# Optimization experiments

Hardware: AMD Instinct MI355X
Metric: run time of the kernel (lower is better)

Reference implementation:

```python
import jax, jax.numpy as jnp
import numpy as np

EPS = 1e-7
POS_THR = 0.5   # max_iou assigner positive threshold
NEG_THR = 0.4   # max_iou assigner negative threshold
ALPHA, GAMMA = 0.25, 2.0  # focal loss defaults


def _rand_boxes(key, shape):
    k1, k2 = jax.random.split(key)
    c = jax.random.uniform(k1, shape + (2,), minval=0.05, maxval=0.95)
    wh = jax.random.uniform(k2, shape + (2,), minval=0.02, maxval=0.3)
    return jnp.concatenate([jnp.clip(c - wh / 2, 0, 1), jnp.clip(c + wh / 2, 0, 1)], -1)


def _grid_anchors():
    # 3 anchor sizes per cell on 80x80, 40x40, 20x20 grids -> 25200 anchors, normalized coords
    boxes = []
    for g, sizes in [(80, (0.04, 0.08, 0.12)), (40, (0.1, 0.2, 0.3)), (20, (0.25, 0.45, 0.65))]:
        c = (np.arange(g, dtype=np.float32) + 0.5) / g
        cx, cy = np.meshgrid(c, c)
        for s in sizes:
            boxes.append(np.stack([cx - s / 2, cy - s / 2, cx + s / 2, cy + s / 2], -1).reshape(-1, 4))
    return jnp.asarray(np.concatenate(boxes, 0), dtype=jnp.float32)


def setup_inputs() -> dict:
    key = jax.random.key(0)
    ks = jax.random.split(key, 6)
    N, P, A, C = 32, 100, 25200, 80
    labels = jax.random.randint(ks[0], (N, P), 0, C)
    y_true = jax.nn.one_hot(labels, C, dtype=jnp.float32)
    bbox_true = _rand_boxes(ks[1], (N, P))
    valid = (jnp.arange(P)[None, :] < 30).astype(jnp.float32)  # 30 real boxes, rest zero-padded
    bbox_true = bbox_true * valid[..., None]
    conf_pred = jax.random.uniform(ks[2], (N, A, 1), minval=0.01, maxval=0.99)
    logit_pred = jax.random.uniform(ks[3], (N, A, C), minval=0.01, maxval=0.99)
    bbox_pred = _rand_boxes(ks[4], (N, A))
    anchors = _grid_anchors()
    return {"y_true": y_true, "bbox_true": bbox_true, "conf_pred": conf_pred,
            "logit_pred": logit_pred, "bbox_pred": bbox_pred, "anchors": anchors}


def pairwise_iou(a, b):
    # a: (A,4), b: (P,4) -> (A,P)
    iw = jnp.clip(jnp.minimum(a[:, None, 2], b[None, :, 2]) - jnp.maximum(a[:, None, 0], b[None, :, 0]), 0)
    ih = jnp.clip(jnp.minimum(a[:, None, 3], b[None, :, 3]) - jnp.maximum(a[:, None, 1], b[None, :, 1]), 0)
    inter = iw * ih
    area_a = (a[:, 2] - a[:, 0]) * (a[:, 3] - a[:, 1])
    area_b = (b[:, 2] - b[:, 0]) * (b[:, 3] - b[:, 1])
    return inter / (area_a[:, None] + area_b[None, :] - inter + EPS)


def target_single(y_true, bbox_true, anchors):
    # mask-based equivalent of the dynamic tf.where/gather/scatter target construction
    P = bbox_true.shape[0]
    valid = jnp.any(bbox_true > 0, axis=-1)  # (P,)
    iou = jnp.where(valid[None, :], pairwise_iou(anchors, bbox_true), -1.0)  # (A,P)
    max_iou = iou.max(-1)
    true_idx = iou.argmax(-1)
    pos = max_iou >= POS_THR
    neg = max_iou < NEG_THR
    # low-quality match: best anchor for each valid gt is positive
    gt_max = iou.max(0)
    gt_best = iou.argmax(0)
    lowq = valid & (gt_max > 0)
    pos = pos.astype(jnp.int32).at[gt_best].max(lowq.astype(jnp.int32)).astype(bool)
    true_idx = true_idx.at[gt_best].set(jnp.where(lowq, jnp.arange(P), true_idx[gt_best]))
    neg = neg & ~pos
    state = jnp.where(pos, 1, jnp.where(neg, -1, 0)).astype(jnp.int8)
    C = y_true.shape[-1]
    background = jnp.zeros((C,), jnp.float32).at[0].set(1.0)  # tf.pad(ones,[0,C-1]) default
    tgt_label = jnp.where(pos[:, None], y_true[true_idx], background[None, :])
    tgt_bbox = jnp.where(pos[:, None], bbox_true[true_idx], 0.0)
    return state[:, None], tgt_label, tgt_bbox


def ciou_loss(bt, bp):
    ix1 = jnp.maximum(bt[..., 0], bp[..., 0]); iy1 = jnp.maximum(bt[..., 1], bp[..., 1])
    ix2 = jnp.minimum(bt[..., 2], bp[..., 2]); iy2 = jnp.minimum(bt[..., 3], bp[..., 3])
    inter = jnp.clip(ix2 - ix1, 0) * jnp.clip(iy2 - iy1, 0)
    wt, ht = bt[..., 2] - bt[..., 0], bt[..., 3] - bt[..., 1]
    wp, hp = bp[..., 2] - bp[..., 0], bp[..., 3] - bp[..., 1]
    union = wt * ht + wp * hp - inter + EPS
    iou = inter / union
    cw = jnp.maximum(bt[..., 2], bp[..., 2]) - jnp.minimum(bt[..., 0], bp[..., 0])
    ch = jnp.maximum(bt[..., 3], bp[..., 3]) - jnp.minimum(bt[..., 1], bp[..., 1])
    c2 = cw * cw + ch * ch + EPS
    rho2 = ((bt[..., 0] + bt[..., 2] - bp[..., 0] - bp[..., 2]) ** 2 +
            (bt[..., 1] + bt[..., 3] - bp[..., 1] - bp[..., 3]) ** 2) / 4.0
    v = (4.0 / (np.pi ** 2)) * (jnp.arctan(wt / (ht + EPS)) - jnp.arctan(wp / (hp + EPS))) ** 2
    alpha = jax.lax.stop_gradient(v / (1.0 - iou + v + EPS))
    return 1.0 - iou + rho2 / c2 + alpha * v


def reference(y_true, bbox_true, conf_pred, logit_pred, bbox_pred, anchors):
    state, t_label, t_bbox = jax.vmap(target_single, in_axes=(0, 0, None))(y_true, bbox_true, anchors)
    dtype = logit_pred.dtype
    pw = (state == 1).astype(dtype)   # positive_weight (N,A,1)
    tw = (state != 0).astype(dtype)   # target_weight   (N,A,1)
    avg_factor = jnp.sum(jnp.maximum(jnp.sum(pw, axis=-2), 1.0))
    # score loss: BCE(positive_weight, conf_pred), weighted by target_weight
    p = jnp.clip(conf_pred, EPS, 1.0 - EPS)
    score_l = -(pw * jnp.log(p) + (1.0 - pw) * jnp.log(1.0 - p))
    score_l = jnp.sum(score_l * tw) / avg_factor
    # class loss: focal BCE, weighted by positive_weight
    q = jnp.clip(logit_pred, EPS, 1.0 - EPS)
    pt = t_label * q + (1.0 - t_label) * (1.0 - q)
    at = t_label * ALPHA + (1.0 - t_label) * (1.0 - ALPHA)
    cls_l = -at * (1.0 - pt) ** GAMMA * jnp.log(pt)
    cls_l = jnp.sum(cls_l * pw) / avg_factor
    # bbox loss: CIoU, weighted by positive_weight
    bl = ciou_loss(t_bbox, bbox_pred)[..., None]
    bbox_l = jnp.sum(bl * pw) / avg_factor
    guard = lambda x: jnp.where(jnp.isnan(x) | jnp.isinf(x), jnp.zeros_like(x), x)  # missing_value=0
    return guard(score_l), guard(cls_l), guard(bbox_l)
```

## Files before the change

kernel.cpp:

```cpp
#include <hip/hip_runtime.h>
#include <math.h>

#define EPSF 1e-7f
#define GCHUNK 10
#define NSEG 8

__device__ __forceinline__ int compact_valid(const float4* __restrict__ bt_n, int P, int tid,
                                             float4* scb, int* sidx, float* sarea, int* wcnt) {
    float4 b = make_float4(0.f, 0.f, 0.f, 0.f);
    bool v = false;
    if (tid < P) {
        b = bt_n[tid];
        v = (b.x > 0.f || b.y > 0.f || b.z > 0.f || b.w > 0.f);
    }
    unsigned long long m = __ballot(v);
    int lane = tid & 63, wv = tid >> 6;
    if (lane == 0) wcnt[wv] = __popcll(m);
    int posn = __popcll(m & ((1ull << lane) - 1ull));
    __syncthreads();
    int base = 0;
    for (int w = 0; w < wv; w++) base += wcnt[w];
    int V = wcnt[0] + wcnt[1] + wcnt[2] + wcnt[3];
    if (v) {
        scb[base + posn] = b;
        sidx[base + posn] = tid;
        sarea[base + posn] = (b.z - b.x) * (b.w - b.y);
    }
    __syncthreads();
    return V;
}

__global__ __launch_bounds__(256) void k_gt_seg(const float4* __restrict__ bbox_true,
                                                const float4* __restrict__ anchors,
                                                float* __restrict__ pn, float* __restrict__ pd,
                                                int* __restrict__ pi,
                                                int N, int P, int A) {
    __shared__ float4 scb[256];
    __shared__ int    sidx[256];
    __shared__ float  sarea[256];
    __shared__ int    wcnt[4];
    __shared__ float  sn[256 * GCHUNK];
    __shared__ float  sd[256 * GCHUNK];
    __shared__ int    si[256 * GCHUNK];

    int n = blockIdx.y, seg = blockIdx.x, tid = threadIdx.x;
    int V = compact_valid(bbox_true + (size_t)n * P, P, tid, scb, sidx, sarea, wcnt);
    int len = (A + NSEG - 1) / NSEG;
    int a0 = seg * len;
    int a1 = a0 + len < A ? a0 + len : A;

    for (int c0 = 0; c0 < V; c0 += GCHUNK) {
        int G = V - c0 < GCHUNK ? V - c0 : GCHUNK;
        float bn[GCHUNK], bd[GCHUNK];
        int   bi[GCHUNK];
#pragma unroll
        for (int g = 0; g < GCHUNK; g++) { bn[g] = -1.f; bd[g] = 1.f; bi[g] = 0x7fffffff; }
        for (int a = a0 + tid; a < a1; a += 256) {
            float4 an = anchors[a];
            float aa = (an.z - an.x) * (an.w - an.y);
#pragma unroll
            for (int g = 0; g < GCHUNK; g++) {
                if (g < G) {
                    float4 b = scb[c0 + g];
                    float iw = fminf(an.z, b.z) - fmaxf(an.x, b.x); iw = iw > 0.f ? iw : 0.f;
                    float ih = fminf(an.w, b.w) - fmaxf(an.y, b.y); ih = ih > 0.f ? ih : 0.f;
                    float inter = iw * ih;
                    float den = aa + sarea[c0 + g] - inter + EPSF;
                    if (inter * bd[g] > bn[g] * den) { bn[g] = inter; bd[g] = den; bi[g] = a; }
                }
            }
        }
        __syncthreads();
#pragma unroll
        for (int g = 0; g < GCHUNK; g++) {
            sn[tid * GCHUNK + g] = bn[g];
            sd[tid * GCHUNK + g] = bd[g];
            si[tid * GCHUNK + g] = bi[g];
        }
        __syncthreads();
        if (tid < G) {
            float Bn = -1.f, Bd = 1.f; int Bi = 0x7fffffff;
            for (int i = 0; i < 256; i++) {
                float cn = sn[i * GCHUNK + tid], cd = sd[i * GCHUNK + tid];
                int ci = si[i * GCHUNK + tid];
                if (cn >= 0.f) {
                    float l = cn * Bd, r = Bn * cd;
                    if (l > r || (l == r && ci < Bi)) { Bn = cn; Bd = cd; Bi = ci; }
                }
            }
            int p = sidx[c0 + tid];
            size_t o = ((size_t)n * P + p) * NSEG + seg;
            pn[o] = Bn; pd[o] = Bd; pi[o] = Bi;
        }
        __syncthreads();
    }
}

__global__ __launch_bounds__(128) void k_merge_scatter(const float4* __restrict__ bbox_true,
                                                       const float* __restrict__ pn,
                                                       const float* __restrict__ pd,
                                                       const int* __restrict__ pi,
                                                       int* __restrict__ ovr,
                                                       int N, int P, int A) {
    int n = blockIdx.x, p = threadIdx.x;
    __shared__ int gb[128];
    __shared__ unsigned char lqs[128];
    if (p < P) {
        float4 b = bbox_true[(size_t)n * P + p];
        bool valid = (b.x > 0.f || b.y > 0.f || b.z > 0.f || b.w > 0.f);
        int g = 0; bool lq = false;
        if (valid) {
            float Bn = -1.f, Bd = 1.f; int Bi = 0x7fffffff;
            const float* qn = pn + ((size_t)n * P + p) * NSEG;
            const float* qd = pd + ((size_t)n * P + p) * NSEG;
            const int*   qi = pi + ((size_t)n * P + p) * NSEG;
            for (int s = 0; s < NSEG; s++) {
                float cn = qn[s], cd = qd[s]; int ci = qi[s];
                if (cn >= 0.f) {
                    float l = cn * Bd, r = Bn * cd;
                    if (l > r || (l == r && ci < Bi)) { Bn = cn; Bd = cd; Bi = ci; }
                }
            }
            g = Bi;
            lq = (Bn > 0.f);
        }
        gb[p] = g; lqs[p] = lq ? 1 : 0;
    }
    __syncthreads();
    if (p < P) {
        int myidx = gb[p];
        bool anylq = false, islast = true;
        for (int q = 0; q < P; q++) {
            if (gb[q] == myidx) {
                if (lqs[q]) anylq = true;
                if (q > p) islast = false;
            }
        }
        if (islast && anylq) ovr[(size_t)n * A + myidx] = lqs[p] ? p : -2;
    }
}

__global__ __launch_bounds__(256) void k_fused(const float4* __restrict__ bbox_true,
                                               const float4* __restrict__ anchors,
                                               const float* __restrict__ conf,
                                               const float* __restrict__ logit,
                                               const float4* __restrict__ bbox_pred,
                                               const float* __restrict__ y_true,
                                               const int* __restrict__ ovr,
                                               double* __restrict__ partial,
                                               int P, int A, int C, int BX) {
    int tid = threadIdx.x;
    int n = blockIdx.y;
    int a = blockIdx.x * blockDim.x + tid;
    int lane = tid & 63, wv = tid >> 6;

    __shared__ float4 scb[256];
    __shared__ int    sidx[256];
    __shared__ float  sarea[256];
    __shared__ int    wcnt[4];

    int V = compact_valid(bbox_true + (size_t)n * P, P, tid, scb, sidx, sarea, wcnt);

    double sc = 0.0, cl = 0.0, bb = 0.0, pc = 0.0;
    if (a < A) {
        float4 an = anchors[a];
        float aa = (an.z - an.x) * (an.w - an.y);
        float bn = -1.f, bd = 1.f; int bi = 0;
        for (int k = 0; k < V; k++) {
            float4 b = scb[k];
            float iw = fminf(an.z, b.z) - fmaxf(an.x, b.x); iw = iw > 0.f ? iw : 0.f;
            float ih = fminf(an.w, b.w) - fmaxf(an.y, b.y); ih = ih > 0.f ? ih : 0.f;
            float inter = iw * ih;
            float den = aa + sarea[k] - inter + EPSF;
            if (inter * bd > bn * den) { bn = inter; bd = den; bi = sidx[k]; }
        }
        bool pos, neg;
        if (V > 0) { pos = (bn >= 0.5f * bd); neg = (bn < 0.4f * bd); }
        else       { pos = false; neg = true; }
        size_t o = (size_t)n * A + a;
        int ov = ovr[o];
        pos = pos || (ov != -1);
        neg = neg && !pos;
        int t = (ov >= 0) ? ov : bi;

        float p = conf[o];
        p = fminf(fmaxf(p, EPSF), 1.f - EPSF);
        if (pos || neg) sc = (double)(pos ? -logf(p) : -logf(1.f - p));
        if (pos) {
            pc = 1.0;
            const float* yt = y_true + ((size_t)n * P + t) * C;
            const float* lg = logit + o * C;
            float s = 0.f;
            for (int c = 0; c < C; c++) {
                float tl = yt[c];
                float q = fminf(fmaxf(lg[c], EPSF), 1.f - EPSF);
                float pt = tl * q + (1.f - tl) * (1.f - q);
                float at = tl * 0.25f + (1.f - tl) * 0.75f;
                float om = 1.f - pt;
                s += -at * om * om * logf(pt);
            }
            cl = (double)s;
            float4 bt = bbox_true[(size_t)n * P + t];
            float4 bp = bbox_pred[o];
            float ix1 = fmaxf(bt.x, bp.x), iy1 = fmaxf(bt.y, bp.y);
            float ix2 = fminf(bt.z, bp.z), iy2 = fminf(bt.w, bp.w);
            float iw = ix2 - ix1; iw = iw > 0.f ? iw : 0.f;
            float ih = iy2 - iy1; ih = ih > 0.f ? ih : 0.f;
            float inter = iw * ih;
            float wt = bt.z - bt.x, ht = bt.w - bt.y;
            float wp = bp.z - bp.x, hp = bp.w - bp.y;
            float uni = wt * ht + wp * hp - inter + EPSF;
            float iou = inter / uni;
            float cw = fmaxf(bt.z, bp.z) - fminf(bt.x, bp.x);
            float ch = fmaxf(bt.w, bp.w) - fminf(bt.y, bp.y);
            float c2 = cw * cw + ch * ch + EPSF;
            float dx = bt.x + bt.z - bp.x - bp.z;
            float dy = bt.y + bt.w - bp.y - bp.w;
            float rho2 = (dx * dx + dy * dy) * 0.25f;
            float dd = atanf(wt / (ht + EPSF)) - atanf(wp / (hp + EPSF));
            float vv = 0.40528473456935109f * dd * dd;
            float al = vv / (1.f - iou + vv + EPSF);
            bb = (double)(1.f - iou + rho2 / c2 + al * vv);
        }
    }

    for (int off = 32; off > 0; off >>= 1) {
        sc += __shfl_down(sc, off, 64);
        cl += __shfl_down(cl, off, 64);
        bb += __shfl_down(bb, off, 64);
        pc += __shfl_down(pc, off, 64);
    }
    __shared__ double sred[4][4];
    if (lane == 0) { sred[wv][0] = sc; sred[wv][1] = cl; sred[wv][2] = bb; sred[wv][3] = pc; }
    __syncthreads();
    if (tid == 0) {
        double r0 = 0, r1 = 0, r2 = 0, r3 = 0;
        for (int w = 0; w < 4; w++) {
            r0 += sred[w][0]; r1 += sred[w][1]; r2 += sred[w][2]; r3 += sred[w][3];
        }
        double* row = partial + ((size_t)n * BX + blockIdx.x) * 4;
        row[0] = r0; row[1] = r1; row[2] = r2; row[3] = r3;
    }
}

__global__ __launch_bounds__(256) void k_final(const double* __restrict__ partial,
                                               float* __restrict__ out, int N, int BX) {
    const int FT = 256;
    int tid = threadIdx.x;
    __shared__ double sh[FT];
    __shared__ double res[3];
    __shared__ double shn[64];

    double s0 = 0, s1 = 0, s2 = 0;
    int total = N * BX;
    for (int i = tid; i < total; i += FT) {
        const double* r = partial + (size_t)i * 4;
        s0 += r[0]; s1 += r[1]; s2 += r[2];
    }
    double vals[3] = {s0, s1, s2};
    for (int k = 0; k < 3; k++) {
        sh[tid] = vals[k];
        __syncthreads();
        for (int s = 128; s > 0; s >>= 1) {
            if (tid < s) sh[tid] += sh[tid + s];
            __syncthreads();
        }
        if (tid == 0) res[k] = sh[0];
        __syncthreads();
    }
    int chunks = FT / N;
    double pcs = 0;
    int n = tid / chunks, c = tid % chunks;
    if (n < N) {
        int per = (BX + chunks - 1) / chunks;
        int j0 = c * per, j1 = (j0 + per < BX) ? j0 + per : BX;
        for (int j = j0; j < j1; j++) pcs += partial[((size_t)n * BX + j) * 4 + 3];
    }
    sh[tid] = pcs;
    __syncthreads();
    if (tid < N) {
        double s = 0;
        for (int c2 = 0; c2 < chunks; c2++) s += sh[tid * chunks + c2];
        shn[tid] = s > 1.0 ? s : 1.0;
    }
    __syncthreads();
    if (tid == 0) {
        double avg = 0;
        for (int i = 0; i < N; i++) avg += shn[i];
        for (int k = 0; k < 3; k++) {
            double x = res[k] / avg;
            if (isnan(x) || isinf(x)) x = 0.0;
            out[k] = (float)x;
        }
    }
}

extern "C" void kernel_launch(void* const* d_in, const int* in_sizes, int n_in,
                              void* d_out, int out_size, void* d_ws, size_t ws_size,
                              hipStream_t stream) {
    const float* y_true    = (const float*)d_in[0];
    const float* bbox_true = (const float*)d_in[1];
    const float* conf      = (const float*)d_in[2];
    const float* logit     = (const float*)d_in[3];
    const float* bboxp     = (const float*)d_in[4];
    const float* anchors   = (const float*)d_in[5];

    int A = in_sizes[5] / 4;
    int N = in_sizes[2] / A;
    int P = in_sizes[1] / (4 * N);
    int C = in_sizes[0] / (N * P);

    int BX = (A + 255) / 256;

    char* w = (char*)d_ws;
    auto alloc = [&](size_t bytes) -> void* {
        void* r = (void*)w;
        w += (bytes + 15) & ~(size_t)15;
        return r;
    };
    int*    ovr     = (int*)alloc(sizeof(int) * (size_t)N * A);
    float*  pn      = (float*)alloc(sizeof(float) * (size_t)N * P * NSEG);
    float*  pd      = (float*)alloc(sizeof(float) * (size_t)N * P * NSEG);
    int*    pi      = (int*)alloc(sizeof(int) * (size_t)N * P * NSEG);
    double* partial = (double*)alloc(sizeof(double) * (size_t)N * BX * 4);

    hipMemsetAsync(ovr, 0xFF, sizeof(int) * (size_t)N * A, stream);

    dim3 gS(NSEG, N);
    k_gt_seg<<<gS, 256, 0, stream>>>((const float4*)bbox_true, (const float4*)anchors,
                                     pn, pd, pi, N, P, A);

    k_merge_scatter<<<N, 128, 0, stream>>>((const float4*)bbox_true, pn, pd, pi,
                                           ovr, N, P, A);

    dim3 gA(BX, N);
    k_fused<<<gA, 256, 0, stream>>>((const float4*)bbox_true, (const float4*)anchors,
                                    conf, logit, (const float4*)bboxp, y_true,
                                    ovr, partial, P, A, C, BX);

    k_final<<<1, 256, 0, stream>>>(partial, (float*)d_out, N, BX);
}
```

Measured before the change: 523.8 us.

## Use wave shuffles for GT argmax, more segments, sparse override list

```diff
diff --git a/kernel.cpp b/kernel.cpp
--- a/kernel.cpp
+++ b/kernel.cpp
@@ -3,7 +3,7 @@
 
 #define EPSF 1e-7f
 #define GCHUNK 10
-#define NSEG 8
+#define NSEG 32
 
 __device__ __forceinline__ int compact_valid(const float4* __restrict__ bt_n, int P, int tid,
                                              float4* scb, int* sidx, float* sarea, int* wcnt) {
@@ -30,7 +30,7 @@
     return V;
 }
 
-__global__ __launch_bounds__(256) void k_gt_seg(const float4* __restrict__ bbox_true,
+__global__ __launch_bounds__(256) void k_gt_all(const float4* __restrict__ bbox_true,
                                                 const float4* __restrict__ anchors,
                                                 float* __restrict__ pn, float* __restrict__ pd,
                                                 int* __restrict__ pi,
@@ -39,11 +39,11 @@
     __shared__ int    sidx[256];
     __shared__ float  sarea[256];
     __shared__ int    wcnt[4];
-    __shared__ float  sn[256 * GCHUNK];
-    __shared__ float  sd[256 * GCHUNK];
-    __shared__ int    si[256 * GCHUNK];
+    __shared__ float  mn[4][GCHUNK], md[4][GCHUNK];
+    __shared__ int    mi[4][GCHUNK];
 
     int n = blockIdx.y, seg = blockIdx.x, tid = threadIdx.x;
+    int lane = tid & 63, wv = tid >> 6;
     int V = compact_valid(bbox_true + (size_t)n * P, P, tid, scb, sidx, sarea, wcnt);
     int len = (A + NSEG - 1) / NSEG;
     int a0 = seg * len;
@@ -70,23 +70,28 @@
                 }
             }
         }
-        __syncthreads();
+        for (int off = 32; off > 0; off >>= 1) {
 #pragma unroll
-        for (int g = 0; g < GCHUNK; g++) {
-            sn[tid * GCHUNK + g] = bn[g];
-            sd[tid * GCHUNK + g] = bd[g];
-            si[tid * GCHUNK + g] = bi[g];
+            for (int g = 0; g < GCHUNK; g++) {
+                float on = __shfl_xor(bn[g], off, 64);
+                float od = __shfl_xor(bd[g], off, 64);
+                int   oi = __shfl_xor(bi[g], off, 64);
+                float l = on * bd[g], r = bn[g] * od;
+                if (l > r || (l == r && oi < bi[g])) { bn[g] = on; bd[g] = od; bi[g] = oi; }
+            }
+        }
+        if (lane == 0) {
+#pragma unroll
+            for (int g = 0; g < GCHUNK; g++) { mn[wv][g] = bn[g]; md[wv][g] = bd[g]; mi[wv][g] = bi[g]; }
         }
         __syncthreads();
         if (tid < G) {
             float Bn = -1.f, Bd = 1.f; int Bi = 0x7fffffff;
-            for (int i = 0; i < 256; i++) {
-                float cn = sn[i * GCHUNK + tid], cd = sd[i * GCHUNK + tid];
-                int ci = si[i * GCHUNK + tid];
-                if (cn >= 0.f) {
-                    float l = cn * Bd, r = Bn * cd;
-                    if (l > r || (l == r && ci < Bi)) { Bn = cn; Bd = cd; Bi = ci; }
-                }
+            for (int w = 0; w < 4; w++) {
+                float cn = mn[w][tid], cd = md[w][tid];
+                int ci = mi[w][tid];
+                float l = cn * Bd, r = Bn * cd;
+                if (l > r || (l == r && ci < Bi)) { Bn = cn; Bd = cd; Bi = ci; }
             }
             int p = sidx[c0 + tid];
             size_t o = ((size_t)n * P + p) * NSEG + seg;
@@ -96,15 +101,18 @@
     }
 }
 
-__global__ __launch_bounds__(128) void k_merge_scatter(const float4* __restrict__ bbox_true,
-                                                       const float* __restrict__ pn,
-                                                       const float* __restrict__ pd,
-                                                       const int* __restrict__ pi,
-                                                       int* __restrict__ ovr,
-                                                       int N, int P, int A) {
+__global__ __launch_bounds__(128) void k_scatter2(const float4* __restrict__ bbox_true,
+                                                  const float* __restrict__ pn,
+                                                  const float* __restrict__ pd,
+                                                  const int* __restrict__ pi,
+                                                  int* __restrict__ ovr_cnt,
+                                                  int2* __restrict__ ovr_list,
+                                                  int N, int P, int A) {
     int n = blockIdx.x, p = threadIdx.x;
     __shared__ int gb[128];
     __shared__ unsigned char lqs[128];
+    __shared__ int cnt;
+    if (p == 0) cnt = 0;
     if (p < P) {
         float4 b = bbox_true[(size_t)n * P + p];
         bool valid = (b.x > 0.f || b.y > 0.f || b.z > 0.f || b.w > 0.f);
@@ -136,8 +144,13 @@
                 if (q > p) islast = false;
             }
         }
-        if (islast && anylq) ovr[(size_t)n * A + myidx] = lqs[p] ? p : -2;
-    }
+        if (islast && anylq) {
+            int s = atomicAdd(&cnt, 1);
+            ovr_list[(size_t)n * P + s] = make_int2(myidx, lqs[p] ? p : -2);
+        }
+    }
+    __syncthreads();
+    if (p == 0) ovr_cnt[n] = cnt;
 }
 
 __global__ __launch_bounds__(256) void k_fused(const float4* __restrict__ bbox_true,
@@ -146,7 +159,8 @@
                                                const float* __restrict__ logit,
                                                const float4* __restrict__ bbox_pred,
                                                const float* __restrict__ y_true,
-                                               const int* __restrict__ ovr,
+                                               const int* __restrict__ ovr_cnt,
+                                               const int2* __restrict__ ovr_list,
                                                double* __restrict__ partial,
                                                int P, int A, int C, int BX) {
     int tid = threadIdx.x;
@@ -158,8 +172,17 @@
     __shared__ int    sidx[256];
     __shared__ float  sarea[256];
     __shared__ int    wcnt[4];
-
+    __shared__ int    sflag[256];
+
+    sflag[tid] = -1;
     int V = compact_valid(bbox_true + (size_t)n * P, P, tid, scb, sidx, sarea, wcnt);
+    int cnt = ovr_cnt[n];
+    if (tid < cnt) {
+        int2 e = ovr_list[(size_t)n * P + tid];
+        int local = e.x - blockIdx.x * 256;
+        if (local >= 0 && local < 256) sflag[local] = e.y;
+    }
+    __syncthreads();
 
     double sc = 0.0, cl = 0.0, bb = 0.0, pc = 0.0;
     if (a < A) {
@@ -177,12 +200,12 @@
         bool pos, neg;
         if (V > 0) { pos = (bn >= 0.5f * bd); neg = (bn < 0.4f * bd); }
         else       { pos = false; neg = true; }
-        size_t o = (size_t)n * A + a;
-        int ov = ovr[o];
+        int ov = sflag[tid];
         pos = pos || (ov != -1);
         neg = neg && !pos;
         int t = (ov >= 0) ? ov : bi;
 
+        size_t o = (size_t)n * A + a;
         float p = conf[o];
         p = fminf(fmaxf(p, EPSF), 1.f - EPSF);
         if (pos || neg) sc = (double)(pos ? -logf(p) : -logf(1.f - p));
@@ -318,25 +341,24 @@
         w += (bytes + 15) & ~(size_t)15;
         return r;
     };
-    int*    ovr     = (int*)alloc(sizeof(int) * (size_t)N * A);
     float*  pn      = (float*)alloc(sizeof(float) * (size_t)N * P * NSEG);
     float*  pd      = (float*)alloc(sizeof(float) * (size_t)N * P * NSEG);
     int*    pi      = (int*)alloc(sizeof(int) * (size_t)N * P * NSEG);
+    int*    ovr_cnt = (int*)alloc(sizeof(int) * (size_t)N);
+    int2*   ovr_list= (int2*)alloc(sizeof(int2) * (size_t)N * P);
     double* partial = (double*)alloc(sizeof(double) * (size_t)N * BX * 4);
 
-    hipMemsetAsync(ovr, 0xFF, sizeof(int) * (size_t)N * A, stream);
-
     dim3 gS(NSEG, N);
-    k_gt_seg<<<gS, 256, 0, stream>>>((const float4*)bbox_true, (const float4*)anchors,
+    k_gt_all<<<gS, 256, 0, stream>>>((const float4*)bbox_true, (const float4*)anchors,
                                      pn, pd, pi, N, P, A);
 
-    k_merge_scatter<<<N, 128, 0, stream>>>((const float4*)bbox_true, pn, pd, pi,
-                                           ovr, N, P, A);
+    k_scatter2<<<N, 128, 0, stream>>>((const float4*)bbox_true, pn, pd, pi,
+                                      ovr_cnt, ovr_list, N, P, A);
 
     dim3 gA(BX, N);
     k_fused<<<gA, 256, 0, stream>>>((const float4*)bbox_true, (const float4*)anchors,
                                     conf, logit, (const float4*)bboxp, y_true,
-                                    ovr, partial, P, A, C, BX);
+                                    ovr_cnt, ovr_list, partial, P, A, C, BX);
 
     k_final<<<1, 256, 0, stream>>>(partial, (float*)d_out, N, BX);
 }
```

Result: faster. 466.3 us (-11.0%).
